# Kernel optimization log

Measured on AMD Instinct MI355X. Metric: run time of the kernel, lower is better.

The kernel has to match this reference:

```python
import jax, jax.numpy as jnp
import numpy as np

B, N, D_IN, D_HID, D_OUT = 4096, 64, 128, 128, 128


def setup_inputs() -> dict:
    key = jax.random.key(0)
    k1, k2, k3, k4, k5, k6 = jax.random.split(key, 6)
    inp = jax.random.normal(k1, (B, D_IN), dtype=jnp.float32)
    neigh = jax.random.normal(k2, (B, N, D_IN), dtype=jnp.float32)
    # zero out some neighbors so the mask path is exercised
    drop = jax.random.bernoulli(k3, 0.2, (B, N))
    neigh = jnp.where(drop[:, :, None], 0.0, neigh)
    W_mlp = jax.random.normal(k4, (D_HID, D_IN), dtype=jnp.float32) * (1.0 / np.sqrt(D_IN))
    b_mlp = jnp.zeros((D_HID,), dtype=jnp.float32)
    W_comb = jax.random.normal(k5, (2 * D_OUT, D_IN + D_HID), dtype=jnp.float32) * (1.0 / np.sqrt(D_IN + D_HID))
    b_comb = jax.random.normal(k6, (2 * D_OUT,), dtype=jnp.float32) * 0.01
    return {"input": inp, "neighbor_inputs": neigh, "W_mlp": W_mlp, "b_mlp": b_mlp,
            "W_comb": W_comb, "b_comb": b_comb}


def reference(input, neighbor_inputs, W_mlp, b_mlp, W_comb, b_comb):
    # mask: neighbors whose features sum to exactly 0 (padding)  [B, N, 1]
    mask = (jnp.sum(neighbor_inputs, axis=-1) == 0.0)[:, :, None]
    # per-neighbor MLP + ReLU: [B, N, D_HID]
    h = jax.nn.relu(jnp.einsum('bnd,hd->bnh', neighbor_inputs, W_mlp) + b_mlp)
    h = jnp.where(mask, 0.0, h)
    # max-pool over neighbor dim -> [B, D_HID]
    pooled = jnp.max(h, axis=1)
    # combine: concat + linear + ReLU -> [B, 2*D_OUT]
    combined = jnp.concatenate([input, pooled], axis=-1)
    out = jax.nn.relu(combined @ W_comb.T + b_comb)
    return out
```

## Files before the change

kernel.cpp:

```cpp
#include <hip/hip_runtime.h>
#include <hip/hip_bf16.h>

typedef __attribute__((ext_vector_type(4))) float f32x4;
typedef __attribute__((ext_vector_type(8))) short bf16x8;

#define N_NEI 64
#define D_IN  128
#define D_HID 128

union BF8 { bf16x8 v; __hip_bfloat162 h[4]; unsigned u[4]; };

__device__ __forceinline__ bf16x8 pack8(const float4& a, const float4& b) {
  BF8 r;
  r.h[0] = __float22bfloat162_rn(float2{a.x, a.y});
  r.h[1] = __float22bfloat162_rn(float2{a.z, a.w});
  r.h[2] = __float22bfloat162_rn(float2{b.x, b.y});
  r.h[3] = __float22bfloat162_rn(float2{b.z, b.w});
  return r.v;
}

__global__ __launch_bounds__(256, 2)
void k1_pool(const float* __restrict__ neigh, const float* __restrict__ Wmlp,
             const float* __restrict__ bmlp, unsigned short* __restrict__ pooled) {
  __shared__ unsigned short Wl[D_HID * D_IN];
  __shared__ float pscr[4][D_HID];

  const int tid = threadIdx.x;
  const int l = tid & 63;
  const int w = tid >> 6;
  const int lr = l & 15;
  const int lg = l >> 4;

  const int b = blockIdx.x * 4 + w;
  const float* rowbase = neigh + (size_t)b * N_NEI * D_IN;

  float4 pf[8];
  {
    const float* arow = rowbase + (size_t)lr * D_IN + lg * 8;
    #pragma unroll
    for (int ks = 0; ks < 4; ++ks) {
      pf[2 * ks]     = *(const float4*)(arow + ks * 32);
      pf[2 * ks + 1] = *(const float4*)(arow + ks * 32 + 4);
    }
  }

  const float4* W4 = (const float4*)Wmlp;
  #pragma unroll
  for (int it = 0; it < 8; ++it) {
    int f8 = it * 256 + tid;
    int j  = f8 >> 4;
    int d0 = (f8 & 15) * 8;
    float4 a = W4[f8 * 2];
    float4 bb = W4[f8 * 2 + 1];
    int byte = j * 256 + ((d0 * 2) ^ ((j & 7) << 4));
    *(bf16x8*)((char*)Wl + byte) = pack8(a, bb);
  }

  float bml[8];
  #pragma unroll
  for (int t = 0; t < 8; ++t) bml[t] = bmlp[t * 16 + lr];

  __syncthreads();

  float pmax[8];
  #pragma unroll
  for (int t = 0; t < 8; ++t) pmax[t] = 0.f;

  #pragma unroll 1
  for (int mt = 0; mt < 4; ++mt) {
    bf16x8 af[4];
    float rs = 0.f;
    #pragma unroll
    for (int ks = 0; ks < 4; ++ks) {
      float4 a0 = pf[2 * ks];
      float4 a1 = pf[2 * ks + 1];
      rs += a0.x + a0.y + a0.z + a0.w + a1.x + a1.y + a1.z + a1.w;
      af[ks] = pack8(a0, a1);
    }

    if (mt < 3) {
      const float* arow = rowbase + (size_t)((mt + 1) * 16 + lr) * D_IN + lg * 8;
      #pragma unroll
      for (int ks = 0; ks < 4; ++ks) {
        pf[2 * ks]     = *(const float4*)(arow + ks * 32);
        pf[2 * ks + 1] = *(const float4*)(arow + ks * 32 + 4);
      }
    }

    rs += __shfl_xor(rs, 16);
    rs += __shfl_xor(rs, 32);
    unsigned mask16 = (unsigned)(__ballot(rs == 0.0f) & 0xFFFFull);

    #pragma unroll 1
    for (int p = 0; p < 2; ++p) {
      f32x4 acc[4];
      #pragma unroll
      for (int tt = 0; tt < 4; ++tt) acc[tt] = (f32x4){0.f, 0.f, 0.f, 0.f};

      #pragma unroll
      for (int tt = 0; tt < 4; ++tt) {
        #pragma unroll
        for (int ks = 0; ks < 4; ++ks) {
          int jr = (p * 4 + tt) * 16 + lr;
          int d0 = ks * 32 + lg * 8;
          bf16x8 bf = *(const bf16x8*)((const char*)Wl + jr * 256 + ((d0 * 2) ^ ((jr & 7) << 4)));
          acc[tt] = __builtin_amdgcn_mfma_f32_16x16x32_bf16(af[ks], bf, acc[tt], 0, 0, 0);
        }
      }

      #pragma unroll
      for (int tt = 0; tt < 4; ++tt) {
        #pragma unroll
        for (int r = 0; r < 4; ++r) {
          int row = lg * 4 + r;
          float v = fmaxf(acc[tt][r] + bml[p * 4 + tt], 0.f);
          if ((mask16 >> row) & 1u) v = 0.f;
          pmax[p * 4 + tt] = fmaxf(pmax[p * 4 + tt], v);
        }
      }
    }
  }

  #pragma unroll
  for (int t = 0; t < 8; ++t) {
    pmax[t] = fmaxf(pmax[t], __shfl_xor(pmax[t], 16));
    pmax[t] = fmaxf(pmax[t], __shfl_xor(pmax[t], 32));
  }

  if (l < 16) {
    #pragma unroll
    for (int t = 0; t < 8; ++t) pscr[w][t * 16 + l] = pmax[t];
  }
  __syncthreads();
  float2 pv = *(const float2*)&pscr[w][2 * l];
  __hip_bfloat162 h2 = __float22bfloat162_rn(pv);
  ((unsigned*)(pooled + (size_t)b * D_HID))[l] = *(unsigned*)&h2;
}

__global__ __launch_bounds__(256, 2)
void k2_comb(const float* __restrict__ inp, const unsigned short* __restrict__ pooled,
             const float* __restrict__ Wcomb, const float* __restrict__ bcomb,
             float* __restrict__ out) {
  __shared__ unsigned short Wl[64 * 256];

  const int tid = threadIdx.x;
  const int l = tid & 63;
  const int w = tid >> 6;
  const int mchunk = blockIdx.x >> 2;
  const int colq   = blockIdx.x & 3;
  const int lr = l & 15;
  const int lg = l >> 4;

  const int row = mchunk * 64 + w * 16 + lr;

  float4 a0[4], a1[4];
  #pragma unroll
  for (int ks = 0; ks < 4; ++ks) {
    const float* p = inp + (size_t)row * 128 + ks * 32 + lg * 8;
    a0[ks] = *(const float4*)p;
    a1[ks] = *(const float4*)(p + 4);
  }
  bf16x8 af[8];
  #pragma unroll
  for (int ks = 4; ks < 8; ++ks) {
    af[ks] = *(const bf16x8*)(pooled + (size_t)row * 128 + (ks - 4) * 32 + lg * 8);
  }

  const float4* W4 = (const float4*)Wcomb;
  #pragma unroll
  for (int it = 0; it < 8; ++it) {
    int c  = it * 256 + tid;
    int jr = c >> 5;
    int d0 = (c & 31) * 8;
    int gidx = ((colq * 64 + jr) * 256 + d0) >> 2;
    float4 a = W4[gidx];
    float4 bb = W4[gidx + 1];
    int byte = jr * 512 + ((d0 * 2) ^ ((jr & 7) << 4));
    *(bf16x8*)((char*)Wl + byte) = pack8(a, bb);
  }

  float bcl[4];
  #pragma unroll
  for (int t = 0; t < 4; ++t) bcl[t] = bcomb[colq * 64 + t * 16 + lr];

  #pragma unroll
  for (int ks = 0; ks < 4; ++ks) af[ks] = pack8(a0[ks], a1[ks]);

  __syncthreads();

  f32x4 acc[4];
  #pragma unroll
  for (int t = 0; t < 4; ++t) acc[t] = (f32x4){0.f, 0.f, 0.f, 0.f};
  #pragma unroll
  for (int t = 0; t < 4; ++t) {
    #pragma unroll
    for (int ks = 0; ks < 8; ++ks) {
      int jr = t * 16 + lr;
      int d0 = ks * 32 + lg * 8;
      bf16x8 bf = *(const bf16x8*)((const char*)Wl + jr * 512 + ((d0 * 2) ^ ((jr & 7) << 4)));
      acc[t] = __builtin_amdgcn_mfma_f32_16x16x32_bf16(af[ks], bf, acc[t], 0, 0, 0);
    }
  }

  #pragma unroll
  for (int t = 0; t < 4; ++t) {
    #pragma unroll
    for (int r = 0; r < 4; ++r) {
      int ro = mchunk * 64 + w * 16 + lg * 4 + r;
      int co = colq * 64 + t * 16 + lr;
      float v = acc[t][r] + bcl[t];
      out[(size_t)ro * 256 + co] = fmaxf(v, 0.f);
    }
  }
}

extern "C" void kernel_launch(void* const* d_in, const int* in_sizes, int n_in,
                              void* d_out, int out_size, void* d_ws, size_t ws_size,
                              hipStream_t stream) {
  const float* inp   = (const float*)d_in[0];
  const float* neigh = (const float*)d_in[1];
  const float* Wmlp  = (const float*)d_in[2];
  const float* bmlp  = (const float*)d_in[3];
  const float* Wcomb = (const float*)d_in[4];
  const float* bcomb = (const float*)d_in[5];
  float* out = (float*)d_out;
  unsigned short* pooled = (unsigned short*)d_ws;

  k1_pool<<<1024, 256, 0, stream>>>(neigh, Wmlp, bmlp, pooled);
  k2_comb<<<256, 256, 0, stream>>>(inp, pooled, Wcomb, bcomb, out);
}
```

Measured before the change: 39.08 us.

## Stream neighbor tiles via async global-to-LDS double buffer and split hidden dim across waves

The pooling kernel now loads each half-batch-row tile (32 neighbors) directly into a double-buffered LDS region using global_load_lds, prefetching the next tile while computing the current one. Work is re-partitioned so each wave owns 32 hidden columns for all neighbors instead of one batch row, letting each block process 8 batch rows with half the grid. The aim is to hide HBM latency for the 128 MB neighbor stream and amortize the weight conversion into LDS over more rows. It adds a block-wide barrier per tile and padded LDS rows, and halves the grid size, which may reduce parallelism.

```diff
diff --git a/kernel.cpp b/kernel.cpp
--- a/kernel.cpp
+++ b/kernel.cpp
@@ -9,6 +9,11 @@
 #define D_HID 128
 
 union BF8 { bf16x8 v; __hip_bfloat162 h[4]; unsigned u[4]; };
+
+__device__ __forceinline__ unsigned bfbits(float f) {
+  unsigned u = __float_as_uint(f);
+  return (u + 0x7fffu + ((u >> 16) & 1u)) >> 16;
+}
 
 __device__ __forceinline__ bf16x8 pack8(const float4& a, const float4& b) {
   BF8 r;
@@ -23,7 +28,7 @@
 void k1_pool(const float* __restrict__ neigh, const float* __restrict__ Wmlp,
              const float* __restrict__ bmlp, unsigned short* __restrict__ pooled) {
   __shared__ unsigned short Wl[D_HID * D_IN];
-  __shared__ float pscr[4][D_HID];
+  __shared__ uint4 Abuf[2][1056];
 
   const int tid = threadIdx.x;
   const int l = tid & 63;
@@ -31,17 +36,15 @@
   const int lr = l & 15;
   const int lg = l >> 4;
 
-  const int b = blockIdx.x * 4 + w;
-  const float* rowbase = neigh + (size_t)b * N_NEI * D_IN;
-
-  float4 pf[8];
-  {
-    const float* arow = rowbase + (size_t)lr * D_IN + lg * 8;
-    #pragma unroll
-    for (int ks = 0; ks < 4; ++ks) {
-      pf[2 * ks]     = *(const float4*)(arow + ks * 32);
-      pf[2 * ks + 1] = *(const float4*)(arow + ks * 32 + 4);
-    }
+  const char* nbase = (const char*)(neigh + (size_t)blockIdx.x * 8 * N_NEI * D_IN);
+
+  #pragma unroll
+  for (int i = 0; i < 4; ++i) {
+    int c = w * 4 + i;
+    __builtin_amdgcn_global_load_lds(
+      (const __attribute__((address_space(1))) unsigned int*)(nbase + c * 1024 + l * 16),
+      (__attribute__((address_space(3))) unsigned int*)((char*)Abuf[0] + c * 1056),
+      16, 0, 0);
   }
 
   const float4* W4 = (const float4*)Wmlp;
@@ -56,85 +59,95 @@
     *(bf16x8*)((char*)Wl + byte) = pack8(a, bb);
   }
 
-  float bml[8];
-  #pragma unroll
-  for (int t = 0; t < 8; ++t) bml[t] = bmlp[t * 16 + lr];
+  const float bml0 = bmlp[w * 32 + lr];
+  const float bml1 = bmlp[w * 32 + 16 + lr];
 
   __syncthreads();
 
-  float pmax[8];
-  #pragma unroll
-  for (int t = 0; t < 8; ++t) pmax[t] = 0.f;
+  float pmax0 = 0.f, pmax1 = 0.f;
 
   #pragma unroll 1
-  for (int mt = 0; mt < 4; ++mt) {
-    bf16x8 af[4];
-    float rs = 0.f;
-    #pragma unroll
-    for (int ks = 0; ks < 4; ++ks) {
-      float4 a0 = pf[2 * ks];
-      float4 a1 = pf[2 * ks + 1];
-      rs += a0.x + a0.y + a0.z + a0.w + a1.x + a1.y + a1.z + a1.w;
-      af[ks] = pack8(a0, a1);
-    }
-
-    if (mt < 3) {
-      const float* arow = rowbase + (size_t)((mt + 1) * 16 + lr) * D_IN + lg * 8;
+  for (int g = 0; g < 16; ++g) {
+    const char* Ab = (const char*)Abuf[g & 1];
+
+    if (g < 15) {
+      const char* src = nbase + (size_t)(g + 1) * 16384;
+      char* dst = (char*)Abuf[(g + 1) & 1];
+      #pragma unroll
+      for (int i = 0; i < 4; ++i) {
+        int c = w * 4 + i;
+        __builtin_amdgcn_global_load_lds(
+          (const __attribute__((address_space(1))) unsigned int*)(src + c * 1024 + l * 16),
+          (__attribute__((address_space(3))) unsigned int*)(dst + c * 1056),
+          16, 0, 0);
+      }
+    }
+
+    bf16x8 af[2][4];
+    float rs0 = 0.f, rs1 = 0.f;
+    #pragma unroll
+    for (int mt = 0; mt < 2; ++mt) {
       #pragma unroll
       for (int ks = 0; ks < 4; ++ks) {
-        pf[2 * ks]     = *(const float4*)(arow + ks * 32);
-        pf[2 * ks + 1] = *(const float4*)(arow + ks * 32 + 4);
-      }
-    }
-
-    rs += __shfl_xor(rs, 16);
-    rs += __shfl_xor(rs, 32);
-    unsigned mask16 = (unsigned)(__ballot(rs == 0.0f) & 0xFFFFull);
-
-    #pragma unroll 1
-    for (int p = 0; p < 2; ++p) {
-      f32x4 acc[4];
-      #pragma unroll
-      for (int tt = 0; tt < 4; ++tt) acc[tt] = (f32x4){0.f, 0.f, 0.f, 0.f};
-
-      #pragma unroll
-      for (int tt = 0; tt < 4; ++tt) {
-        #pragma unroll
-        for (int ks = 0; ks < 4; ++ks) {
-          int jr = (p * 4 + tt) * 16 + lr;
-          int d0 = ks * 32 + lg * 8;
-          bf16x8 bf = *(const bf16x8*)((const char*)Wl + jr * 256 + ((d0 * 2) ^ ((jr & 7) << 4)));
-          acc[tt] = __builtin_amdgcn_mfma_f32_16x16x32_bf16(af[ks], bf, acc[tt], 0, 0, 0);
-        }
-      }
-
-      #pragma unroll
-      for (int tt = 0; tt < 4; ++tt) {
-        #pragma unroll
-        for (int r = 0; r < 4; ++r) {
-          int row = lg * 4 + r;
-          float v = fmaxf(acc[tt][r] + bml[p * 4 + tt], 0.f);
-          if ((mask16 >> row) & 1u) v = 0.f;
-          pmax[p * 4 + tt] = fmaxf(pmax[p * 4 + tt], v);
-        }
-      }
-    }
-  }
-
-  #pragma unroll
-  for (int t = 0; t < 8; ++t) {
-    pmax[t] = fmaxf(pmax[t], __shfl_xor(pmax[t], 16));
-    pmax[t] = fmaxf(pmax[t], __shfl_xor(pmax[t], 32));
-  }
-
-  if (l < 16) {
-    #pragma unroll
-    for (int t = 0; t < 8; ++t) pscr[w][t * 16 + l] = pmax[t];
-  }
-  __syncthreads();
-  float2 pv = *(const float2*)&pscr[w][2 * l];
-  __hip_bfloat162 h2 = __float22bfloat162_rn(pv);
-  ((unsigned*)(pooled + (size_t)b * D_HID))[l] = *(unsigned*)&h2;
+        int r = mt * 16 + lr;
+        int addr = (r >> 1) * 1056 + (r & 1) * 512 + ks * 128 + lg * 32;
+        float4 a0 = *(const float4*)(Ab + addr);
+        float4 a1 = *(const float4*)(Ab + addr + 16);
+        float s = a0.x + a0.y + a0.z + a0.w + a1.x + a1.y + a1.z + a1.w;
+        if (mt == 0) rs0 += s; else rs1 += s;
+        af[mt][ks] = pack8(a0, a1);
+      }
+    }
+    rs0 += __shfl_xor(rs0, 16); rs0 += __shfl_xor(rs0, 32);
+    rs1 += __shfl_xor(rs1, 16); rs1 += __shfl_xor(rs1, 32);
+    unsigned mask0 = (unsigned)(__ballot(rs0 == 0.0f) & 0xFFFFull);
+    unsigned mask1 = (unsigned)(__ballot(rs1 == 0.0f) & 0xFFFFull);
+
+    f32x4 acc[2][2];
+    acc[0][0] = (f32x4){0.f, 0.f, 0.f, 0.f};
+    acc[0][1] = (f32x4){0.f, 0.f, 0.f, 0.f};
+    acc[1][0] = (f32x4){0.f, 0.f, 0.f, 0.f};
+    acc[1][1] = (f32x4){0.f, 0.f, 0.f, 0.f};
+    #pragma unroll
+    for (int nt = 0; nt < 2; ++nt) {
+      #pragma unroll
+      for (int ks = 0; ks < 4; ++ks) {
+        int jr = w * 32 + nt * 16 + lr;
+        int d0 = ks * 32 + lg * 8;
+        bf16x8 bf = *(const bf16x8*)((const char*)Wl + jr * 256 + ((d0 * 2) ^ ((jr & 7) << 4)));
+        acc[0][nt] = __builtin_amdgcn_mfma_f32_16x16x32_bf16(af[0][ks], bf, acc[0][nt], 0, 0, 0);
+        acc[1][nt] = __builtin_amdgcn_mfma_f32_16x16x32_bf16(af[1][ks], bf, acc[1][nt], 0, 0, 0);
+      }
+    }
+
+    #pragma unroll
+    for (int mt = 0; mt < 2; ++mt) {
+      unsigned m = mt ? mask1 : mask0;
+      #pragma unroll
+      for (int r = 0; r < 4; ++r) {
+        int row = lg * 4 + r;
+        bool msk = (m >> row) & 1u;
+        float v0 = fmaxf(acc[mt][0][r] + bml0, 0.f);
+        float v1 = fmaxf(acc[mt][1][r] + bml1, 0.f);
+        if (msk) { v0 = 0.f; v1 = 0.f; }
+        pmax0 = fmaxf(pmax0, v0);
+        pmax1 = fmaxf(pmax1, v1);
+      }
+    }
+
+    if (g & 1) {
+      float p0 = fmaxf(pmax0, __shfl_xor(pmax0, 16)); p0 = fmaxf(p0, __shfl_xor(p0, 32));
+      float p1 = fmaxf(pmax1, __shfl_xor(pmax1, 16)); p1 = fmaxf(p1, __shfl_xor(p1, 32));
+      if (lg == 0) {
+        size_t bb = (size_t)blockIdx.x * 8 + (g >> 1);
+        pooled[bb * D_HID + w * 32 + lr]      = (unsigned short)bfbits(p0);
+        pooled[bb * D_HID + w * 32 + 16 + lr] = (unsigned short)bfbits(p1);
+      }
+      pmax0 = 0.f; pmax1 = 0.f;
+    }
+
+    __syncthreads();
+  }
 }
 
 __global__ __launch_bounds__(256, 2)
@@ -226,6 +239,6 @@
   float* out = (float*)d_out;
   unsigned short* pooled = (unsigned short*)d_ws;
 
-  k1_pool<<<1024, 256, 0, stream>>>(neigh, Wmlp, bmlp, pooled);
+  k1_pool<<<512, 256, 0, stream>>>(neigh, Wmlp, bmlp, pooled);
   k2_comb<<<256, 256, 0, stream>>>(inp, pooled, Wcomb, bcomb, out);
 }
```

New measurement: 75.69 us. 1.94x slower.

## Split hidden dim across two waves per batch row, keep W_mlp fragments in registers

Applied to the files above, without the earlier changes.

Each batch row's 128 hidden units are now split between two waves, so the pool kernel launches twice as many blocks. Each wave loads its 64-column half of W_mlp directly from global into bf16 MFMA fragments held in registers. This removes the 32KB shared-memory staging, the block barrier and the LDS reads in the inner loop. The trade-off is that the neighbor tile is read twice (once per half), roughly doubling global traffic on the dominant input. Register pressure also rises from the 16 held weight fragments.

```diff
diff --git a/kernel.cpp b/kernel.cpp
--- a/kernel.cpp
+++ b/kernel.cpp
@@ -9,6 +9,11 @@
 #define D_HID 128
 
 union BF8 { bf16x8 v; __hip_bfloat162 h[4]; unsigned u[4]; };
+
+__device__ __forceinline__ unsigned bfbits(float f) {
+  unsigned u = __float_as_uint(f);
+  return (u + 0x7fffu + ((u >> 16) & 1u)) >> 16;
+}
 
 __device__ __forceinline__ bf16x8 pack8(const float4& a, const float4& b) {
   BF8 r;
@@ -22,49 +27,45 @@
 __global__ __launch_bounds__(256, 2)
 void k1_pool(const float* __restrict__ neigh, const float* __restrict__ Wmlp,
              const float* __restrict__ bmlp, unsigned short* __restrict__ pooled) {
-  __shared__ unsigned short Wl[D_HID * D_IN];
-  __shared__ float pscr[4][D_HID];
-
   const int tid = threadIdx.x;
   const int l = tid & 63;
   const int w = tid >> 6;
   const int lr = l & 15;
   const int lg = l >> 4;
 
-  const int b = blockIdx.x * 4 + w;
+  const int gw = blockIdx.x * 4 + w;
+  const int b    = gw >> 1;
+  const int half = gw & 1;
+
   const float* rowbase = neigh + (size_t)b * N_NEI * D_IN;
 
   float4 pf[8];
   {
-    const float* arow = rowbase + (size_t)lr * D_IN + lg * 8;
+    const float* ra = rowbase + (size_t)lr * D_IN + lg * 8;
     #pragma unroll
     for (int ks = 0; ks < 4; ++ks) {
-      pf[2 * ks]     = *(const float4*)(arow + ks * 32);
-      pf[2 * ks + 1] = *(const float4*)(arow + ks * 32 + 4);
-    }
-  }
-
-  const float4* W4 = (const float4*)Wmlp;
-  #pragma unroll
-  for (int it = 0; it < 8; ++it) {
-    int f8 = it * 256 + tid;
-    int j  = f8 >> 4;
-    int d0 = (f8 & 15) * 8;
-    float4 a = W4[f8 * 2];
-    float4 bb = W4[f8 * 2 + 1];
-    int byte = j * 256 + ((d0 * 2) ^ ((j & 7) << 4));
-    *(bf16x8*)((char*)Wl + byte) = pack8(a, bb);
-  }
-
-  float bml[8];
-  #pragma unroll
-  for (int t = 0; t < 8; ++t) bml[t] = bmlp[t * 16 + lr];
-
-  __syncthreads();
-
-  float pmax[8];
-  #pragma unroll
-  for (int t = 0; t < 8; ++t) pmax[t] = 0.f;
+      pf[2 * ks]     = *(const float4*)(ra + ks * 32);
+      pf[2 * ks + 1] = *(const float4*)(ra + ks * 32 + 4);
+    }
+  }
+
+  bf16x8 bfr[4][4];
+  #pragma unroll
+  for (int t = 0; t < 4; ++t) {
+    #pragma unroll
+    for (int ks = 0; ks < 4; ++ks) {
+      const float* wp = Wmlp + (size_t)(half * 64 + t * 16 + lr) * D_IN + ks * 32 + lg * 8;
+      float4 w0 = *(const float4*)wp;
+      float4 w1 = *(const float4*)(wp + 4);
+      bfr[t][ks] = pack8(w0, w1);
+    }
+  }
+
+  float bml[4];
+  #pragma unroll
+  for (int t = 0; t < 4; ++t) bml[t] = bmlp[half * 64 + t * 16 + lr];
+
+  float pmax[4] = {0.f, 0.f, 0.f, 0.f};
 
   #pragma unroll 1
   for (int mt = 0; mt < 4; ++mt) {
@@ -79,11 +80,11 @@
     }
 
     if (mt < 3) {
-      const float* arow = rowbase + (size_t)((mt + 1) * 16 + lr) * D_IN + lg * 8;
+      const float* ra = rowbase + (size_t)((mt + 1) * 16 + lr) * D_IN + lg * 8;
       #pragma unroll
       for (int ks = 0; ks < 4; ++ks) {
-        pf[2 * ks]     = *(const float4*)(arow + ks * 32);
-        pf[2 * ks + 1] = *(const float4*)(arow + ks * 32 + 4);
+        pf[2 * ks]     = *(const float4*)(ra + ks * 32);
+        pf[2 * ks + 1] = *(const float4*)(ra + ks * 32 + 4);
       }
     }
 
@@ -91,50 +92,39 @@
     rs += __shfl_xor(rs, 32);
     unsigned mask16 = (unsigned)(__ballot(rs == 0.0f) & 0xFFFFull);
 
-    #pragma unroll 1
-    for (int p = 0; p < 2; ++p) {
-      f32x4 acc[4];
+    f32x4 acc[4];
+    #pragma unroll
+    for (int t = 0; t < 4; ++t) acc[t] = (f32x4){0.f, 0.f, 0.f, 0.f};
+    #pragma unroll
+    for (int t = 0; t < 4; ++t) {
       #pragma unroll
-      for (int tt = 0; tt < 4; ++tt) acc[tt] = (f32x4){0.f, 0.f, 0.f, 0.f};
-
+      for (int ks = 0; ks < 4; ++ks) {
+        acc[t] = __builtin_amdgcn_mfma_f32_16x16x32_bf16(af[ks], bfr[t][ks], acc[t], 0, 0, 0);
+      }
+    }
+
+    #pragma unroll
+    for (int t = 0; t < 4; ++t) {
       #pragma unroll
-      for (int tt = 0; tt < 4; ++tt) {
-        #pragma unroll
-        for (int ks = 0; ks < 4; ++ks) {
-          int jr = (p * 4 + tt) * 16 + lr;
-          int d0 = ks * 32 + lg * 8;
-          bf16x8 bf = *(const bf16x8*)((const char*)Wl + jr * 256 + ((d0 * 2) ^ ((jr & 7) << 4)));
-          acc[tt] = __builtin_amdgcn_mfma_f32_16x16x32_bf16(af[ks], bf, acc[tt], 0, 0, 0);
-        }
+      for (int r = 0; r < 4; ++r) {
+        int row = lg * 4 + r;
+        float v = fmaxf(acc[t][r] + bml[t], 0.f);
+        if ((mask16 >> row) & 1u) v = 0.f;
+        pmax[t] = fmaxf(pmax[t], v);
       }
-
-      #pragma unroll
-      for (int tt = 0; tt < 4; ++tt) {
-        #pragma unroll
-        for (int r = 0; r < 4; ++r) {
-          int row = lg * 4 + r;
-          float v = fmaxf(acc[tt][r] + bml[p * 4 + tt], 0.f);
-          if ((mask16 >> row) & 1u) v = 0.f;
-          pmax[p * 4 + tt] = fmaxf(pmax[p * 4 + tt], v);
-        }
-      }
-    }
-  }
-
-  #pragma unroll
-  for (int t = 0; t < 8; ++t) {
+    }
+  }
+
+  #pragma unroll
+  for (int t = 0; t < 4; ++t) {
     pmax[t] = fmaxf(pmax[t], __shfl_xor(pmax[t], 16));
     pmax[t] = fmaxf(pmax[t], __shfl_xor(pmax[t], 32));
   }
-
   if (l < 16) {
-    #pragma unroll
-    for (int t = 0; t < 8; ++t) pscr[w][t * 16 + l] = pmax[t];
-  }
-  __syncthreads();
-  float2 pv = *(const float2*)&pscr[w][2 * l];
-  __hip_bfloat162 h2 = __float22bfloat162_rn(pv);
-  ((unsigned*)(pooled + (size_t)b * D_HID))[l] = *(unsigned*)&h2;
+    unsigned short* pp = pooled + (size_t)b * D_HID + half * 64;
+    #pragma unroll
+    for (int t = 0; t < 4; ++t) pp[t * 16 + l] = (unsigned short)bfbits(pmax[t]);
+  }
 }
 
 __global__ __launch_bounds__(256, 2)
@@ -226,6 +216,6 @@
   float* out = (float*)d_out;
   unsigned short* pooled = (unsigned short*)d_ws;
 
-  k1_pool<<<1024, 256, 0, stream>>>(neigh, Wmlp, bmlp, pooled);
+  k1_pool<<<2048, 256, 0, stream>>>(neigh, Wmlp, bmlp, pooled);
   k2_comb<<<256, 256, 0, stream>>>(inp, pooled, Wcomb, bcomb, out);
 }
```

Measured after the change: 68.04 us. 1.74x slower.

## Stream neighbor tiles into LDS via async global_load_lds double buffering

Applied to the files above, without the earlier changes.

The pooling kernel now has each wave process four batch rows instead of one, cutting the grid from 1024 to 256 blocks so the per-block W_mlp conversion into LDS is amortised over more work. Neighbor features are copied straight from global memory into a per-wave, double-buffered, padded LDS tile with async global-to-LDS loads, prefetching the next 16-neighbor tile while the MFMAs run on the current one. The pooled result is flushed every four steps. In exchange, the extra LDS drops occupancy to one block per CU, and the compiler may insert full memory waits before the LDS reads, which would serialise the prefetch.

```diff
diff --git a/kernel.cpp b/kernel.cpp
--- a/kernel.cpp
+++ b/kernel.cpp
@@ -9,6 +9,11 @@
 #define D_HID 128
 
 union BF8 { bf16x8 v; __hip_bfloat162 h[4]; unsigned u[4]; };
+
+__device__ __forceinline__ unsigned bfbits(float f) {
+  unsigned u = __float_as_uint(f);
+  return (u + 0x7fffu + ((u >> 16) & 1u)) >> 16;
+}
 
 __device__ __forceinline__ bf16x8 pack8(const float4& a, const float4& b) {
   BF8 r;
@@ -19,10 +24,11 @@
   return r.v;
 }
 
-__global__ __launch_bounds__(256, 2)
+__global__ __launch_bounds__(256, 1)
 void k1_pool(const float* __restrict__ neigh, const float* __restrict__ Wmlp,
              const float* __restrict__ bmlp, unsigned short* __restrict__ pooled) {
   __shared__ unsigned short Wl[D_HID * D_IN];
+  __shared__ __align__(16) char Abuf[4][2][8 * 1040];
   __shared__ float pscr[4][D_HID];
 
   const int tid = threadIdx.x;
@@ -31,17 +37,15 @@
   const int lr = l & 15;
   const int lg = l >> 4;
 
-  const int b = blockIdx.x * 4 + w;
-  const float* rowbase = neigh + (size_t)b * N_NEI * D_IN;
-
-  float4 pf[8];
-  {
-    const float* arow = rowbase + (size_t)lr * D_IN + lg * 8;
-    #pragma unroll
-    for (int ks = 0; ks < 4; ++ks) {
-      pf[2 * ks]     = *(const float4*)(arow + ks * 32);
-      pf[2 * ks + 1] = *(const float4*)(arow + ks * 32 + 4);
-    }
+  const int brow0 = blockIdx.x * 16 + w * 4;
+  const char* wsrc = (const char*)(neigh + (size_t)brow0 * N_NEI * D_IN);
+
+  #pragma unroll
+  for (int i = 0; i < 8; ++i) {
+    __builtin_amdgcn_global_load_lds(
+      (const __attribute__((address_space(1))) unsigned int*)(wsrc + i * 1024 + l * 16),
+      (__attribute__((address_space(3))) unsigned int*)(&Abuf[w][0][0] + i * 1040),
+      16, 0, 0);
   }
 
   const float4* W4 = (const float4*)Wmlp;
@@ -67,26 +71,30 @@
   for (int t = 0; t < 8; ++t) pmax[t] = 0.f;
 
   #pragma unroll 1
-  for (int mt = 0; mt < 4; ++mt) {
+  for (int s = 0; s < 16; ++s) {
+    if (s < 15) {
+      const char* src = wsrc + (size_t)(s + 1) * 8192;
+      char* dst = &Abuf[w][(s + 1) & 1][0];
+      #pragma unroll
+      for (int i = 0; i < 8; ++i) {
+        __builtin_amdgcn_global_load_lds(
+          (const __attribute__((address_space(1))) unsigned int*)(src + i * 1024 + l * 16),
+          (__attribute__((address_space(3))) unsigned int*)(dst + i * 1040),
+          16, 0, 0);
+      }
+    }
+
+    const char* Ab = &Abuf[w][s & 1][0];
     bf16x8 af[4];
     float rs = 0.f;
     #pragma unroll
     for (int ks = 0; ks < 4; ++ks) {
-      float4 a0 = pf[2 * ks];
-      float4 a1 = pf[2 * ks + 1];
+      int ad = (lr >> 1) * 1040 + (lr & 1) * 512 + ks * 128 + lg * 32;
+      float4 a0 = *(const float4*)(Ab + ad);
+      float4 a1 = *(const float4*)(Ab + ad + 16);
       rs += a0.x + a0.y + a0.z + a0.w + a1.x + a1.y + a1.z + a1.w;
       af[ks] = pack8(a0, a1);
     }
-
-    if (mt < 3) {
-      const float* arow = rowbase + (size_t)((mt + 1) * 16 + lr) * D_IN + lg * 8;
-      #pragma unroll
-      for (int ks = 0; ks < 4; ++ks) {
-        pf[2 * ks]     = *(const float4*)(arow + ks * 32);
-        pf[2 * ks + 1] = *(const float4*)(arow + ks * 32 + 4);
-      }
-    }
-
     rs += __shfl_xor(rs, 16);
     rs += __shfl_xor(rs, 32);
     unsigned mask16 = (unsigned)(__ballot(rs == 0.0f) & 0xFFFFull);
@@ -119,22 +127,24 @@
         }
       }
     }
-  }
-
-  #pragma unroll
-  for (int t = 0; t < 8; ++t) {
-    pmax[t] = fmaxf(pmax[t], __shfl_xor(pmax[t], 16));
-    pmax[t] = fmaxf(pmax[t], __shfl_xor(pmax[t], 32));
-  }
-
-  if (l < 16) {
-    #pragma unroll
-    for (int t = 0; t < 8; ++t) pscr[w][t * 16 + l] = pmax[t];
-  }
-  __syncthreads();
-  float2 pv = *(const float2*)&pscr[w][2 * l];
-  __hip_bfloat162 h2 = __float22bfloat162_rn(pv);
-  ((unsigned*)(pooled + (size_t)b * D_HID))[l] = *(unsigned*)&h2;
+
+    if ((s & 3) == 3) {
+      #pragma unroll
+      for (int t = 0; t < 8; ++t) {
+        pmax[t] = fmaxf(pmax[t], __shfl_xor(pmax[t], 16));
+        pmax[t] = fmaxf(pmax[t], __shfl_xor(pmax[t], 32));
+      }
+      if (l < 16) {
+        #pragma unroll
+        for (int t = 0; t < 8; ++t) pscr[w][t * 16 + l] = pmax[t];
+      }
+      float2 pv = *(const float2*)&pscr[w][2 * l];
+      __hip_bfloat162 h2 = __float22bfloat162_rn(pv);
+      ((unsigned*)(pooled + (size_t)(brow0 + (s >> 2)) * D_HID))[l] = *(unsigned*)&h2;
+      #pragma unroll
+      for (int t = 0; t < 8; ++t) pmax[t] = 0.f;
+    }
+  }
 }
 
 __global__ __launch_bounds__(256, 2)
@@ -226,6 +236,6 @@
   float* out = (float*)d_out;
   unsigned short* pooled = (unsigned short*)d_ws;
 
-  k1_pool<<<1024, 256, 0, stream>>>(neigh, Wmlp, bmlp, pooled);
+  k1_pool<<<256, 256, 0, stream>>>(neigh, Wmlp, bmlp, pooled);
   k2_comb<<<256, 256, 0, stream>>>(inp, pooled, Wcomb, bcomb, out);
 }
```

Result: slower. 56.12 us (+43.6%).
